# Kernel tuning notes

Measured on AMD Instinct MI355X. Metric: run time of the kernel, lower is better.

The kernel has to match this reference:

```python
import jax, jax.numpy as jnp
from jax import lax
import numpy as np

# label LUT: 36 raw labels -> 20 classes (from the module's labmap dict)
LUT = jnp.array(list(range(20)) + [1,2,3,4,5,6,7,8,9,10,14,15,16,17,18,19], dtype=jnp.int32)
R = 20  # kernel radius = ceil(truncated(4) * max sigma(5)); static for jit


def _gauss_kernel(sigma):
    k = jnp.arange(-R, R + 1, dtype=jnp.float32)
    w = jnp.exp(-0.5 * (k / sigma) ** 2)
    return w / jnp.sum(w)


def _smooth_axis(vol, w, axis):
    # vol: [D,H,W]; separable 1D zero-padded convolution along `axis`
    v = jnp.moveaxis(vol, axis, -1)
    sh = v.shape
    v2 = v.reshape(-1, 1, sh[-1])                      # [N,1,L]
    out = lax.conv_general_dilated(v2, w.reshape(1, 1, -1), (1,), [(R, R)])
    return jnp.moveaxis(out.reshape(sh), -1, axis)


def _gsmooth3(vol, sigma):
    # vol: [D,H,W]
    w = _gauss_kernel(sigma)
    for ax in range(3):
        vol = _smooth_axis(vol, w, ax)
    return vol


def setup_inputs() -> dict:
    key = jax.random.key(0)
    ks = jax.random.split(key, 6)
    shape = (1, 128, 160, 128)
    x = jax.random.randint(ks[0], shape, 0, 36, dtype=jnp.int32)
    noise = jax.random.normal(ks[1], (20,) + shape, dtype=jnp.float32)
    mus = jax.random.uniform(ks[2], (20,), minval=0.0, maxval=255.0, dtype=jnp.float32)
    stds = jax.random.uniform(ks[3], (20,), minval=0.0, maxval=16.0, dtype=jnp.float32)
    gmm_sigmas = jax.random.uniform(ks[4], (20,), minval=0.1, maxval=5.0, dtype=jnp.float32)
    final_sigma = jax.random.uniform(ks[5], (), minval=0.1, maxval=5.0, dtype=jnp.float32)
    return {"x": x, "noise": noise, "mus": mus, "stds": stds,
            "gmm_sigmas": gmm_sigmas, "final_sigma": final_sigma}


def reference(x, noise, mus, stds, gmm_sigmas, final_sigma):
    # 1) vectorized LUT remap (replaces the sequential tensor.apply_)
    xr = LUT[x[0]]                                      # [D,H,W] int32
    # 2) per-class masked Gaussian noise fields: (mu_i + std_i * N(0,1)) * (xr == i)
    classes = jnp.arange(20, dtype=jnp.int32)
    masks = (xr[None] == classes[:, None, None, None]).astype(jnp.float32)  # [20,D,H,W]
    fields = (mus[:, None, None, None] + stds[:, None, None, None] * noise[:, 0]) * masks
    # 3) per-class Gaussian smoothing (vmapped over the 20 classes), then sum
    smoothed = jax.vmap(_gsmooth3)(fields, gmm_sigmas)  # [20,D,H,W]
    summed = jnp.sum(smoothed, axis=0)                  # [D,H,W]
    # 4) final Gaussian smooth
    out = _gsmooth3(summed, final_sigma)
    return out[None]                                    # [1,D,H,W]
```

## Files before the change

kernel.cpp:

```cpp
#include <hip/hip_runtime.h>

constexpr int DD = 128, HH = 160, WW = 128;
constexpr int ZSTR = HH * WW;
constexpr long long NV = (long long)DD * HH * WW;
constexpr long long VOLB = NV * 4;
constexpr int RAD = 20, NTAP = 41;
constexpr int PW = 176;
constexpr int PADC = 24;
constexpr long long NVP = (long long)DD * HH * PW;

__device__ __forceinline__ int lutmap(int v) {
    return v < 20 ? v : (v < 30 ? v - 19 : v - 16);
}

__device__ __forceinline__ void taps(const float* win, const float* __restrict__ w,
                                     float acc[8]) {
#pragma unroll
    for (int k = 0; k < NTAP; ++k) {
        float wk = w[k];
#pragma unroll
        for (int p = 0; p < 8; ++p) acc[p] = fmaf(wk, win[k + p], acc[p]);
    }
}

__global__ __launch_bounds__(256) void kprep2(const int* __restrict__ x,
                                              const float* __restrict__ noise,
                                              const float* __restrict__ mus,
                                              const float* __restrict__ stds,
                                              float* __restrict__ vp,
                                              unsigned char* __restrict__ cp) {
    int z = blockIdx.y;
    int idx = blockIdx.x * 256 + threadIdx.x;
    int y = idx / PW, xp = idx - y * PW;
    long long po = (long long)z * HH * PW + idx;
    int gx = xp - PADC;
    if ((unsigned)gx < (unsigned)WW) {
        long long gi = (long long)z * ZSTR + (long long)y * WW + gx;
        int c = lutmap(x[gi]);
        vp[po] = mus[c] + stds[c] * noise[(long long)c * NV + gi];
        cp[po] = (unsigned char)c;
    } else {
        vp[po] = 0.f;
        cp[po] = (unsigned char)255;
    }
}

__global__ __launch_bounds__(256) void kpad(const float* __restrict__ src,
                                            float* __restrict__ vp) {
    int z = blockIdx.y;
    int idx = blockIdx.x * 256 + threadIdx.x;
    int y = idx / PW, xp = idx - y * PW;
    long long po = (long long)z * HH * PW + idx;
    int gx = xp - PADC;
    vp[po] = ((unsigned)gx < (unsigned)WW)
                 ? src[(long long)z * ZSTR + (long long)y * WW + gx]
                 : 0.f;
}

__global__ void kweights(const float* __restrict__ gsig, const float* __restrict__ fsig,
                         float* __restrict__ wts) {
    int c = threadIdx.x;
    if (c > 20) return;
    float sigma = (c < 20) ? gsig[c] : fsig[0];
    float inv = 1.0f / sigma;
    float buf[NTAP];
    float s = 0.f;
    for (int k = 0; k < NTAP; ++k) {
        float d = (float)(k - RAD) * inv;
        buf[k] = expf(-0.5f * d * d);
        s += buf[k];
    }
    float r = 1.0f / s;
    for (int k = 0; k < NTAP; ++k) wts[c * NTAP + k] = buf[k] * r;
}

template <bool MASKED>
__global__ __launch_bounds__(256, 4) void ksmooth_xy2(const float* __restrict__ vp,
                                                      const unsigned char* __restrict__ cp,
                                                      const float* __restrict__ wts,
                                                      float* __restrict__ dst, int c0) {
    __shared__ float A2[208][33];

    const int cls_i = MASKED ? (c0 + (int)blockIdx.x) : 20;
    const int x0 = (int)blockIdx.y * 32;
    const int z = blockIdx.z;
    const float* __restrict__ w = wts + cls_i * NTAP;
    const int tid = threadIdx.x;

    for (int i = tid; i < 48 * 32; i += 256) {
        int r = i >> 5, xx = i & 31;
        A2[(r < 24) ? r : (160 + r)][xx] = 0.f;
    }

    const long long zb = (long long)z * HH * PW;
    const int m = tid & 3, q = tid >> 2, xb = m * 8;
#pragma unroll
    for (int pass = 0; pass < 3; ++pass) {
        int y = pass * 64 + q;
        if (y < HH) {
            const float* srcp = vp + zb + (long long)y * PW + (x0 + xb + 4);
            float win[48];
            if (MASKED) {
                const unsigned* cu =
                    (const unsigned*)(cp + zb + (long long)y * PW + (x0 + xb + 4));
                const unsigned cb = (unsigned)cls_i;
#pragma unroll
                for (int i = 0; i < 12; ++i) {
                    float4 v4 = ((const float4*)srcp)[i];
                    unsigned u = cu[i];
                    win[4 * i + 0] = ((u & 0xffu) == cb) ? v4.x : 0.f;
                    win[4 * i + 1] = (((u >> 8) & 0xffu) == cb) ? v4.y : 0.f;
                    win[4 * i + 2] = (((u >> 16) & 0xffu) == cb) ? v4.z : 0.f;
                    win[4 * i + 3] = ((u >> 24) == cb) ? v4.w : 0.f;
                }
            } else {
#pragma unroll
                for (int i = 0; i < 12; ++i) {
                    float4 v4 = ((const float4*)srcp)[i];
                    win[4 * i + 0] = v4.x;
                    win[4 * i + 1] = v4.y;
                    win[4 * i + 2] = v4.z;
                    win[4 * i + 3] = v4.w;
                }
            }
            float acc[8] = {0, 0, 0, 0, 0, 0, 0, 0};
            taps(win, w, acc);
#pragma unroll
            for (int p = 0; p < 8; ++p) A2[24 + y][xb + p] = acc[p];
        }
    }
    __syncthreads();

    const int x = tid & 31, yg = tid >> 5;
    const long long obase =
        (MASKED ? ((long long)blockIdx.x * DD + z) : (long long)z) * ZSTR;
#pragma unroll
    for (int pass = 0; pass < 3; ++pass) {
        int yb = pass * 64 + yg * 8;
        if (yb < HH) {
            float win[48];
#pragma unroll
            for (int j = 0; j < 48; ++j) win[j] = A2[yb + 4 + j][x];
            float acc[8] = {0, 0, 0, 0, 0, 0, 0, 0};
            taps(win, w, acc);
#pragma unroll
            for (int p = 0; p < 8; ++p)
                dst[obase + (long long)(yb + p) * WW + x0 + x] = acc[p];
        }
    }
}

template <bool ACCUM>
__global__ __launch_bounds__(256) void ksmooth_z3(const float* __restrict__ src,
                                                  const float* __restrict__ wts,
                                                  float* __restrict__ out, int c0,
                                                  int nc) {
    __shared__ float L[2][168][17];

    const int x0 = (int)blockIdx.x * 16;
    const int y = (int)blockIdx.y;
    const int tid = threadIdx.x;
    const int sxq = tid & 3;
    const int szr = tid >> 2;
    const int cx = tid & 15;
    const int tg = tid >> 4;
    const int zb = tg * 8;

    const long long colbase = (long long)y * WW + x0;
    const long long sgoff = colbase + sxq * 4;

    for (int i = tid; i < 2 * 40 * 16; i += 256) {
        int b = i / 640;
        int rem = i - b * 640;
        int r = rem >> 4, col = rem & 15;
        L[b][(r < 20) ? r : (128 + r)][col] = 0.f;
    }

    {
        const float4 va = *(const float4*)(src + (long long)szr * ZSTR + sgoff);
        const float4 vb = *(const float4*)(src + (long long)(szr + 64) * ZSTR + sgoff);
        const int wc = sxq * 4;
        L[0][20 + szr][wc + 0] = va.x;
        L[0][20 + szr][wc + 1] = va.y;
        L[0][20 + szr][wc + 2] = va.z;
        L[0][20 + szr][wc + 3] = va.w;
        L[0][84 + szr][wc + 0] = vb.x;
        L[0][84 + szr][wc + 1] = vb.y;
        L[0][84 + szr][wc + 2] = vb.z;
        L[0][84 + szr][wc + 3] = vb.w;
    }
    __syncthreads();

    float acc[8] = {0, 0, 0, 0, 0, 0, 0, 0};
    for (int cc = 0; cc < nc; ++cc) {
        const int cur = cc & 1;
        const bool more = (cc + 1 < nc);
        float4 na, nb;
        if (more) {
            const float* sv = src + (long long)(cc + 1) * NV;
            na = *(const float4*)(sv + (long long)szr * ZSTR + sgoff);
            nb = *(const float4*)(sv + (long long)(szr + 64) * ZSTR + sgoff);
        }
        {
            const float* w = wts + (ACCUM ? (c0 + cc) : 20) * NTAP;
            float win[48];
#pragma unroll
            for (int j = 0; j < 48; ++j) win[j] = L[cur][zb + j][cx];
            taps(win, w, acc);
        }
        if (more) {
            const int nxt = cur ^ 1;
            const int wc = sxq * 4;
            L[nxt][20 + szr][wc + 0] = na.x;
            L[nxt][20 + szr][wc + 1] = na.y;
            L[nxt][20 + szr][wc + 2] = na.z;
            L[nxt][20 + szr][wc + 3] = na.w;
            L[nxt][84 + szr][wc + 0] = nb.x;
            L[nxt][84 + szr][wc + 1] = nb.y;
            L[nxt][84 + szr][wc + 2] = nb.z;
            L[nxt][84 + szr][wc + 3] = nb.w;
        }
        __syncthreads();
    }

#pragma unroll
    for (int p = 0; p < 8; ++p) {
        long long o = (long long)(zb + p) * ZSTR + colbase + cx;
        if (ACCUM)
            out[o] += acc[p];
        else
            out[o] = acc[p];
    }
}

extern "C" void kernel_launch(void* const* d_in, const int* in_sizes, int n_in,
                              void* d_out, int out_size, void* d_ws, size_t ws_size,
                              hipStream_t stream) {
    const int* x = (const int*)d_in[0];
    const float* noise = (const float*)d_in[1];
    const float* mus = (const float*)d_in[2];
    const float* stds = (const float*)d_in[3];
    const float* gsig = (const float*)d_in[4];
    const float* fsig = (const float*)d_in[5];
    float* out = (float*)d_out;

    char* ws = (char*)d_ws;
    size_t off = 0;
    float* wts = (float*)(ws + off);
    off += 4096;
    float* vp = (float*)(ws + off);
    off += (size_t)(NVP * 4);
    unsigned char* cpv = (unsigned char*)(ws + off);
    off += (size_t)NVP;
    float* xy = (float*)(ws + off);
    float* ftmp = xy;

    long long cap = ((long long)ws_size - (long long)off) / VOLB;
    int C = cap < 1 ? 1 : (cap > 20 ? 20 : (int)cap);

    kweights<<<1, 64, 0, stream>>>(gsig, fsig, wts);
    kprep2<<<dim3(HH * PW / 256, DD), 256, 0, stream>>>(x, noise, mus, stds, vp, cpv);
    hipMemsetAsync(d_out, 0, (size_t)VOLB, stream);

    for (int c0 = 0; c0 < 20; c0 += C) {
        int cc = (20 - c0) < C ? (20 - c0) : C;
        ksmooth_xy2<true><<<dim3(cc, 4, DD), 256, 0, stream>>>(vp, cpv, wts, xy, c0);
        ksmooth_z3<true><<<dim3(WW / 16, HH), 256, 0, stream>>>(xy, wts, out, c0, cc);
    }
    kpad<<<dim3(HH * PW / 256, DD), 256, 0, stream>>>(out, vp);
    ksmooth_xy2<false><<<dim3(1, 4, DD), 256, 0, stream>>>(vp, cpv, wts, ftmp, 0);
    ksmooth_z3<false><<<dim3(WW / 16, HH), 256, 0, stream>>>(ftmp, wts, out, 0, 1);
}
```

Before: 535.1 us.

## Transpose xy intermediate to y-major layout, vectorize prep, fuse padding into z pass

The xy-smoothing kernel now writes its intermediate in a [y][z][x] layout, so the z-smoothing kernel reads contiguous z rows for a fixed y instead of striding by a full plane. The prep kernel handles four voxels per thread with int4/float4 loads and packed class bytes. When the workspace holds all 20 classes, the z pass writes straight into the padded buffer, which removes the memset and the kpad launch. This uses an extra volume of workspace and adds a second code path.

```diff
diff --git a/kernel.cpp b/kernel.cpp
--- a/kernel.cpp
+++ b/kernel.cpp
@@ -8,6 +8,7 @@
 constexpr int PW = 176;
 constexpr int PADC = 24;
 constexpr long long NVP = (long long)DD * HH * PW;
+constexpr int PV4 = HH * PW / 4;
 
 __device__ __forceinline__ int lutmap(int v) {
     return v < 20 ? v : (v < 30 ? v - 19 : v - 16);
@@ -23,26 +24,39 @@
     }
 }
 
-__global__ __launch_bounds__(256) void kprep2(const int* __restrict__ x,
-                                              const float* __restrict__ noise,
-                                              const float* __restrict__ mus,
-                                              const float* __restrict__ stds,
-                                              float* __restrict__ vp,
-                                              unsigned char* __restrict__ cp) {
-    int z = blockIdx.y;
-    int idx = blockIdx.x * 256 + threadIdx.x;
-    int y = idx / PW, xp = idx - y * PW;
-    long long po = (long long)z * HH * PW + idx;
-    int gx = xp - PADC;
+__global__ __launch_bounds__(256) void kprep2v(const int* __restrict__ x,
+                                               const float* __restrict__ noise,
+                                               const float* __restrict__ mus,
+                                               const float* __restrict__ stds,
+                                               float* __restrict__ vp,
+                                               unsigned* __restrict__ cp4) {
+    const int z = blockIdx.y;
+    const int t = blockIdx.x * 256 + threadIdx.x;
+    if (t >= PV4) return;
+    const int col4 = t * 4;
+    const int y = col4 / PW;
+    const int xp = col4 - y * PW;
+    const long long o4 = (long long)z * PV4 + t;
+    const int gx = xp - PADC;
+    float4 v;
+    unsigned cw;
     if ((unsigned)gx < (unsigned)WW) {
-        long long gi = (long long)z * ZSTR + (long long)y * WW + gx;
-        int c = lutmap(x[gi]);
-        vp[po] = mus[c] + stds[c] * noise[(long long)c * NV + gi];
-        cp[po] = (unsigned char)c;
+        const long long gi = (long long)z * ZSTR + (long long)y * WW + gx;
+        const int4 xv = *(const int4*)(x + gi);
+        const int c0 = lutmap(xv.x), c1 = lutmap(xv.y), c2 = lutmap(xv.z),
+                  c3 = lutmap(xv.w);
+        v.x = mus[c0] + stds[c0] * noise[(long long)c0 * NV + gi];
+        v.y = mus[c1] + stds[c1] * noise[(long long)c1 * NV + gi + 1];
+        v.z = mus[c2] + stds[c2] * noise[(long long)c2 * NV + gi + 2];
+        v.w = mus[c3] + stds[c3] * noise[(long long)c3 * NV + gi + 3];
+        cw = (unsigned)c0 | ((unsigned)c1 << 8) | ((unsigned)c2 << 16) |
+             ((unsigned)c3 << 24);
     } else {
-        vp[po] = 0.f;
-        cp[po] = (unsigned char)255;
-    }
+        v = make_float4(0.f, 0.f, 0.f, 0.f);
+        cw = 0xFFFFFFFFu;
+    }
+    ((float4*)vp)[o4] = v;
+    cp4[o4] = cw;
 }
 
 __global__ __launch_bounds__(256) void kpad(const float* __restrict__ src,
@@ -132,8 +146,7 @@
     __syncthreads();
 
     const int x = tid & 31, yg = tid >> 5;
-    const long long obase =
-        (MASKED ? ((long long)blockIdx.x * DD + z) : (long long)z) * ZSTR;
+    const long long vbase = MASKED ? ((long long)blockIdx.x * HH) : 0LL;
 #pragma unroll
     for (int pass = 0; pass < 3; ++pass) {
         int yb = pass * 64 + yg * 8;
@@ -145,13 +158,13 @@
             taps(win, w, acc);
 #pragma unroll
             for (int p = 0; p < 8; ++p)
-                dst[obase + (long long)(yb + p) * WW + x0 + x] = acc[p];
-        }
-    }
-}
-
-template <bool ACCUM>
-__global__ __launch_bounds__(256) void ksmooth_z3(const float* __restrict__ src,
+                dst[((vbase + yb + p) * DD + z) * WW + x0 + x] = acc[p];
+        }
+    }
+}
+
+template <int MODE>
+__global__ __launch_bounds__(256) void ksmooth_z4(const float* __restrict__ src,
                                                   const float* __restrict__ wts,
                                                   float* __restrict__ out, int c0,
                                                   int nc) {
@@ -166,8 +179,7 @@
     const int tg = tid >> 4;
     const int zb = tg * 8;
 
-    const long long colbase = (long long)y * WW + x0;
-    const long long sgoff = colbase + sxq * 4;
+    const long long ybase = (long long)y * DD * WW + x0 + sxq * 4;
 
     for (int i = tid; i < 2 * 40 * 16; i += 256) {
         int b = i / 640;
@@ -177,8 +189,8 @@
     }
 
     {
-        const float4 va = *(const float4*)(src + (long long)szr * ZSTR + sgoff);
-        const float4 vb = *(const float4*)(src + (long long)(szr + 64) * ZSTR + sgoff);
+        const float4 va = *(const float4*)(src + ybase + (long long)szr * WW);
+        const float4 vb = *(const float4*)(src + ybase + (long long)(szr + 64) * WW);
         const int wc = sxq * 4;
         L[0][20 + szr][wc + 0] = va.x;
         L[0][20 + szr][wc + 1] = va.y;
@@ -198,11 +210,11 @@
         float4 na, nb;
         if (more) {
             const float* sv = src + (long long)(cc + 1) * NV;
-            na = *(const float4*)(sv + (long long)szr * ZSTR + sgoff);
-            nb = *(const float4*)(sv + (long long)(szr + 64) * ZSTR + sgoff);
+            na = *(const float4*)(sv + ybase + (long long)szr * WW);
+            nb = *(const float4*)(sv + ybase + (long long)(szr + 64) * WW);
         }
         {
-            const float* w = wts + (ACCUM ? (c0 + cc) : 20) * NTAP;
+            const float* w = wts + ((MODE == 1) ? 20 : (c0 + cc)) * NTAP;
             float win[48];
 #pragma unroll
             for (int j = 0; j < 48; ++j) win[j] = L[cur][zb + j][cx];
@@ -225,11 +237,16 @@
 
 #pragma unroll
     for (int p = 0; p < 8; ++p) {
-        long long o = (long long)(zb + p) * ZSTR + colbase + cx;
-        if (ACCUM)
-            out[o] += acc[p];
-        else
-            out[o] = acc[p];
+        const int zo = zb + p;
+        if (MODE == 0) {
+            out[(long long)zo * HH * PW + (long long)y * PW + PADC + x0 + cx] = acc[p];
+        } else {
+            long long o = (long long)zo * ZSTR + (long long)y * WW + x0 + cx;
+            if (MODE == 2)
+                out[o] += acc[p];
+            else
+                out[o] = acc[p];
+        }
     }
 }
 
@@ -252,22 +269,31 @@
     off += (size_t)(NVP * 4);
     unsigned char* cpv = (unsigned char*)(ws + off);
     off += (size_t)NVP;
+    float* ftmp = (float*)(ws + off);
+    off += (size_t)VOLB;
     float* xy = (float*)(ws + off);
-    float* ftmp = xy;
 
     long long cap = ((long long)ws_size - (long long)off) / VOLB;
     int C = cap < 1 ? 1 : (cap > 20 ? 20 : (int)cap);
 
     kweights<<<1, 64, 0, stream>>>(gsig, fsig, wts);
-    kprep2<<<dim3(HH * PW / 256, DD), 256, 0, stream>>>(x, noise, mus, stds, vp, cpv);
-    hipMemsetAsync(d_out, 0, (size_t)VOLB, stream);
-
-    for (int c0 = 0; c0 < 20; c0 += C) {
-        int cc = (20 - c0) < C ? (20 - c0) : C;
-        ksmooth_xy2<true><<<dim3(cc, 4, DD), 256, 0, stream>>>(vp, cpv, wts, xy, c0);
-        ksmooth_z3<true><<<dim3(WW / 16, HH), 256, 0, stream>>>(xy, wts, out, c0, cc);
-    }
-    kpad<<<dim3(HH * PW / 256, DD), 256, 0, stream>>>(out, vp);
-    ksmooth_xy2<false><<<dim3(1, 4, DD), 256, 0, stream>>>(vp, cpv, wts, ftmp, 0);
-    ksmooth_z3<false><<<dim3(WW / 16, HH), 256, 0, stream>>>(ftmp, wts, out, 0, 1);
-}
+    kprep2v<<<dim3((PV4 + 255) / 256, DD), 256, 0, stream>>>(x, noise, mus, stds, vp,
+                                                             (unsigned*)cpv);
+
+    if (C >= 20) {
+        ksmooth_xy2<true><<<dim3(20, 4, DD), 256, 0, stream>>>(vp, cpv, wts, xy, 0);
+        ksmooth_z4<0><<<dim3(WW / 16, HH), 256, 0, stream>>>(xy, wts, vp, 0, 20);
+        ksmooth_xy2<false><<<dim3(1, 4, DD), 256, 0, stream>>>(vp, cpv, wts, ftmp, 0);
+        ksmooth_z4<1><<<dim3(WW / 16, HH), 256, 0, stream>>>(ftmp, wts, out, 0, 1);
+    } else {
+        hipMemsetAsync(d_out, 0, (size_t)VOLB, stream);
+        for (int c0 = 0; c0 < 20; c0 += C) {
+            int cc = (20 - c0) < C ? (20 - c0) : C;
+            ksmooth_xy2<true><<<dim3(cc, 4, DD), 256, 0, stream>>>(vp, cpv, wts, xy, c0);
+            ksmooth_z4<2><<<dim3(WW / 16, HH), 256, 0, stream>>>(xy, wts, out, c0, cc);
+        }
+        kpad<<<dim3(HH * PW / 256, DD), 256, 0, stream>>>(out, vp);
+        ksmooth_xy2<false><<<dim3(1, 4, DD), 256, 0, stream>>>(vp, cpv, wts, ftmp, 0);
+        ksmooth_z4<1><<<dim3(WW / 16, HH), 256, 0, stream>>>(ftmp, wts, out, 0, 1);
+    }
+}
```

Result: faster. 524.3 us (-2.0%).
